# Kernel optimization log

Hardware: AMD Instinct MI355X
Metric: run time of the kernel (lower is better)

The kernel has to match this reference:

```python
import jax, jax.numpy as jnp
import numpy as np

IMG = 640
STRIDES = (8, 16, 32)
A = 5            # anchors per level
NC = 80          # num classes
IOU_TH = 0.5
NEG_RATIO = 1.0


def make_priors():
    scales = [1.0, 1.5, 2.0, 2.5, 3.0]
    out = []
    for s in STRIDES:
        f = IMG // s
        ys, xs = np.meshgrid(np.arange(f), np.arange(f), indexing='ij')
        cx = ((xs + 0.5) / f).ravel()
        cy = ((ys + 0.5) / f).ravel()
        for sc in scales:  # anchor-major to match merge_features (A, h, w) order
            wh = min(sc * 4.0 * s / IMG, 1.0)
            out.append(np.stack([cx, cy, np.full_like(cx, wh), np.full_like(cx, wh)], 1))
    return np.concatenate(out, 0).astype(np.float32)  # [42000, 4] cxcywh


def merge_features(feats):
    outs = []
    for feat in feats:
        n, c, h, w = feat.shape
        f = feat.reshape(n, A, c // A, h, w).transpose(0, 1, 3, 4, 2)
        outs.append(f.reshape(n, A * h * w, c // A))
    return jnp.concatenate(outs, axis=1)  # [n, M, 85]


def box_iou_cxcywh(a, b):
    # a [T,4], b [M,4] (cx,cy,w,h) -> IoU [T,M]
    a1 = jnp.concatenate([a[:, :2] - a[:, 2:] / 2, a[:, :2] + a[:, 2:] / 2], -1)
    b1 = jnp.concatenate([b[:, :2] - b[:, 2:] / 2, b[:, :2] + b[:, 2:] / 2], -1)
    tl = jnp.maximum(a1[:, None, :2], b1[None, :, :2])
    br = jnp.minimum(a1[:, None, 2:], b1[None, :, 2:])
    wh = jnp.clip(br - tl, 0.0)
    inter = wh[..., 0] * wh[..., 1]
    area_a = a[:, 2] * a[:, 3]
    area_b = b[:, 2] * b[:, 3]
    return inter / (area_a[:, None] + area_b[None, :] - inter + 1e-9)


def build_targets(targets, priors, batch):
    ious = box_iou_cxcywh(targets[:, 2:6], priors)  # [Nt, M]
    Nt, M = ious.shape
    img_ids = targets[:, 0].astype(jnp.int32)

    def per_image(i):
        valid = img_ids == i  # [Nt]
        iv = jnp.where(valid[:, None], ious, -1.0)
        best_gt_overlap = iv.max(0)            # [M]
        best_gt_idx = iv.argmax(0)             # [M]
        best_prior_idx = iv.argmax(1)          # [Nt]
        # torch: index_fill_(1) then sequential best_gt_overlap[best_prior_idx[j]] = j
        local_j = (jnp.cumsum(valid.astype(jnp.int32)) - 1).astype(jnp.float32)
        scat_idx = jnp.where(valid, best_prior_idx, M)  # drop invalid rows
        best_gt_overlap = best_gt_overlap.at[scat_idx].set(local_j, mode='drop')
        bbox = targets[best_gt_idx, 2:6]
        clss = targets[best_gt_idx, 1] + 1.0
        clss = jnp.where(best_gt_overlap < IOU_TH, 0.0, clss)
        t_xy = (bbox[:, :2] - priors[:, :2]) / priors[:, 2:]
        t_wh = jnp.log(bbox[:, 2:] / priors[:, 2:])
        return t_xy, t_wh, clss

    return jax.vmap(per_image)(jnp.arange(batch))  # [B,M,2],[B,M,2],[B,M]


def _smooth_l1(x):
    ax = jnp.abs(x)
    return jnp.where(ax < 1.0, 0.5 * ax * ax, ax - 0.5)


def compute_loss(preds, priors, targets):
    n, m, _ = preds.shape
    t_xy, t_wh, t_cls = build_targets(targets, priors, n)
    pos = t_cls > 0
    posf = pos.astype(preds.dtype)
    num_pos = posf.sum()

    # lbox: smooth L1 on xy and wh over positives (mean over pos*2 elements each)
    den2 = jnp.maximum(num_pos * 2.0, 1.0)
    lbox = (_smooth_l1(preds[..., 0:2] - t_xy) * posf[..., None]).sum() / den2 \
         + (_smooth_l1(preds[..., 2:4] - t_wh) * posf[..., None]).sum() / den2

    # lcls: cross entropy over positives, labels = t_cls - 1
    labels = jnp.clip(t_cls.astype(jnp.int32) - 1, 0, NC - 1)
    logz = jax.nn.log_softmax(preds[..., 5:], axis=-1)
    ce = -jnp.take_along_axis(logz, labels[..., None], axis=-1)[..., 0]
    lcls = (ce * posf).sum() / jnp.maximum(num_pos, 1.0)

    # hard negative mining (no grad): double argsort rank trick
    obj = preds[..., 4]
    loss_c = jax.lax.stop_gradient(-jax.nn.log_sigmoid(obj))
    loss_c = jnp.where(pos, 0.0, loss_c)
    order = jnp.argsort(-loss_c, axis=-1)
    rank = jnp.argsort(order, axis=-1)
    num_neg = jnp.minimum(NEG_RATIO * num_pos, m - num_pos)
    neg = rank.astype(preds.dtype) < num_neg
    sel = (pos | neg).astype(preds.dtype)

    # lobj: BCE-with-logits over pos|neg
    z = posf
    bce = jnp.maximum(obj, 0.0) - obj * z + jnp.log1p(jnp.exp(-jnp.abs(obj)))
    lobj = (bce * sel).sum() / jnp.maximum(sel.sum(), 1.0)

    loss = lbox + lcls + lobj
    return jnp.stack([loss, lbox, lobj, lcls])


def setup_inputs() -> dict:
    key = jax.random.key(0)
    ks = jax.random.split(key, 6)
    feat0 = jax.random.normal(ks[0], (8, 425, 80, 80), jnp.float32)
    feat1 = jax.random.normal(ks[1], (8, 425, 40, 40), jnp.float32)
    feat2 = jax.random.normal(ks[2], (8, 425, 20, 20), jnp.float32)
    B, T = 8, 20
    img = jnp.repeat(jnp.arange(B, dtype=jnp.float32), T)
    cls = jax.random.randint(ks[3], (B * T,), 0, NC).astype(jnp.float32)
    cxcy = jax.random.uniform(ks[4], (B * T, 2), minval=0.2, maxval=0.8)
    wh = jax.random.uniform(ks[5], (B * T, 2), minval=0.05, maxval=0.3)
    targets = jnp.concatenate([img[:, None], cls[:, None], cxcy, wh], 1)
    priors = jnp.asarray(make_priors())
    return {"feat0": feat0, "feat1": feat1, "feat2": feat2,
            "targets": targets, "priors": priors}


def reference(feat0, feat1, feat2, targets, priors):
    preds = merge_features([feat0, feat1, feat2])  # [8, 42000, 85]
    return compute_loss(preds, priors, targets)    # [loss, lbox, lobj, lcls]
```

## Files before the change

kernel.cpp:

```cpp
#include <hip/hip_runtime.h>
#include <math.h>

#define MTOT 42000
#define NB 8
#define NCLS 80
#define CAP_LIST 4096
#define MAXT 256
#define NT_MAX 2048
#define GX_MAIN 165
#define NBLK_MAIN (GX_MAIN*NB)
#define NBLK_SEL 1313
#define NCH 32
#define CS 1313

#define O_OVR 0
#define O_GIX (O_OVR + NB*MTOT*4)
#define O_LSC (O_GIX + NB*MTOT*4)
#define O_BCE (O_LSC + NB*MTOT*4)
#define O_BPI (O_BCE + NB*MTOT*4)
#define O_LJ  (O_BPI + NT_MAX*4)
#define O_LST (O_LJ + NT_MAX*4)
#define O_BPP (O_LST + NB*MAXT*4)
#define O_PA  (O_BPP + NT_MAX*NCH*8)
#define O_PN  (O_PA + NBLK_MAIN*16)
#define O_P2  (O_PN + NBLK_MAIN*4)
#define O_BINL (O_P2 + NBLK_SEL*8)
#define O_HA  (O_BINL + NB*CAP_LIST*2*4)
#define O_HB  (O_HA + NB*256*4)
#define O_ACC (O_HB + NB*256*4)
#define O_ACCI (O_ACC + 64)
#define O_CNT (O_ACCI + 256)
#define O_ZEND (O_CNT + 64)

__device__ __forceinline__ float iou_cxcywh(float acx,float acy,float aw,float ah,
                                            float bcx,float bcy,float bw,float bh){
  float ax0=acx-aw*0.5f, ay0=acy-ah*0.5f, ax1=acx+aw*0.5f, ay1=acy+ah*0.5f;
  float bx0=bcx-bw*0.5f, by0=bcy-bh*0.5f, bx1=bcx+bw*0.5f, by1=bcy+bh*0.5f;
  float tlx=fmaxf(ax0,bx0), tly=fmaxf(ay0,by0);
  float brx=fminf(ax1,bx1), bry=fminf(ay1,by1);
  float wx=fmaxf(brx-tlx,0.f), wy=fmaxf(bry-tly,0.f);
  float inter=wx*wy;
  return inter/(aw*ah+bw*bh-inter+1e-9f);
}

__device__ __forceinline__ float sl1(float x){
  float ax=fabsf(x); return ax<1.f ? 0.5f*ax*ax : ax-0.5f;
}

__device__ __forceinline__ void feat_base(const float* f0,const float* f1,const float* f2,
                                          int i,int m,const float** basep,int* hwp){
  const float* fp; int hw, loc;
  if(m<32000){ fp=f0; hw=6400; loc=m; }
  else if(m<40000){ fp=f1; hw=1600; loc=m-32000; }
  else { fp=f2; hw=400; loc=m-40000; }
  int a=loc/hw, p=loc-a*hw;
  *basep = fp + (size_t)(i*425 + a*85)*(size_t)hw + p;
  *hwp = hw;
}

__global__ void k_prep(const float* __restrict__ tg, int nt, int* __restrict__ list,
                       int* __restrict__ cnt, int* __restrict__ lj){
  int t=blockIdx.x*blockDim.x+threadIdx.x;
  if(t>=nt) return;
  int img=(int)tg[t*6];
  int j=0;
  for(int q=0;q<t;q++) if((int)tg[q*6]==img) j++;
  lj[t]=j;
  if(img>=0 && img<NB){
    atomicAdd(&cnt[img],1);
    if(j<MAXT) list[img*MAXT+j]=t;
  }
}

__global__ void k_match(const float* __restrict__ tg, const float* __restrict__ priors,
                        const int* __restrict__ list, const int* __restrict__ cnt,
                        float* __restrict__ ovr, int* __restrict__ gix){
  __shared__ float st[MAXT*6];
  __shared__ int   sidx[MAXT];
  int i = blockIdx.y;
  int n = min(cnt[i],MAXT);
  for(int j=threadIdx.x;j<n;j+=blockDim.x){
    int t=list[i*MAXT+j];
    sidx[j]=t;
    #pragma unroll
    for(int q=0;q<6;q++) st[j*6+q]=tg[t*6+q];
  }
  __syncthreads();
  int m = blockIdx.x*blockDim.x + threadIdx.x;
  if(m>=MTOT) return;
  float4 pr = ((const float4*)priors)[m];
  float maxv=-1.0f; int bi=0;
  for(int j=0;j<n;j++){
    float v=iou_cxcywh(st[j*6+2],st[j*6+3],st[j*6+4],st[j*6+5], pr.x,pr.y,pr.z,pr.w);
    if(v>maxv){ maxv=v; bi=sidx[j]; }
  }
  ovr[i*MTOT+m]=maxv; gix[i*MTOT+m]=bi;
}

__global__ void k_bpA(const float* __restrict__ tg, const float* __restrict__ priors,
                      int nt, unsigned long long* __restrict__ part){
  __shared__ unsigned long long s[256];
  int t=blockIdx.y; if(t>=nt) return;
  int c=blockIdx.x;
  float acx=tg[t*6+2],acy=tg[t*6+3],aw=tg[t*6+4],ah=tg[t*6+5];
  int m0=c*CS, m1=min(m0+CS,MTOT);
  float bv=-1.f; int bm=0;
  for(int m=m0+threadIdx.x;m<m1;m+=blockDim.x){
    float4 pr=((const float4*)priors)[m];
    float v=iou_cxcywh(acx,acy,aw,ah,pr.x,pr.y,pr.z,pr.w);
    if(v>bv){ bv=v; bm=m; }
  }
  unsigned long long p = (bv<0.f) ? 0ull
      : (((unsigned long long)__float_as_uint(bv))<<32) | (unsigned)(~bm);
  s[threadIdx.x]=p;
  __syncthreads();
  for(int o=128;o>0;o>>=1){
    if(threadIdx.x<o){ if(s[threadIdx.x+o]>s[threadIdx.x]) s[threadIdx.x]=s[threadIdx.x+o]; }
    __syncthreads();
  }
  if(threadIdx.x==0) part[(size_t)t*NCH+c]=s[0];
}

__global__ void k_bpB(const unsigned long long* __restrict__ part, int nt,
                      int* __restrict__ bpi){
  __shared__ unsigned long long s[64];
  int t=blockIdx.x; if(t>=nt) return;
  int l=threadIdx.x;
  s[l]=(l<NCH)? part[(size_t)t*NCH+l] : 0ull;
  __syncthreads();
  for(int o=32;o>0;o>>=1){
    if(l<o){ if(s[l+o]>s[l]) s[l]=s[l+o]; }
    __syncthreads();
  }
  if(l==0) bpi[t]=~((unsigned)(s[0]&0xFFFFFFFFull));
}

__global__ void k_scatter(const float* __restrict__ tg, int nt,
                          const int* __restrict__ bpi, const int* __restrict__ lj,
                          float* __restrict__ ovr){
  int t=blockIdx.x*blockDim.x+threadIdx.x;
  if(t>=nt) return;
  int img=(int)tg[t*6];
  if(img<0||img>=NB) return;
  int myp=bpi[t];
  for(int q=t+1;q<nt;q++)
    if((int)tg[q*6]==img && bpi[q]==myp) return;
  ovr[img*MTOT+myp]=(float)lj[t];
}

__global__ void k_main(const float* __restrict__ f0,const float* __restrict__ f1,const float* __restrict__ f2,
                       const float* __restrict__ tg,const float* __restrict__ priors,
                       const float* __restrict__ ovr,const int* __restrict__ gix,
                       float* __restrict__ lsc,float* __restrict__ bcearr,
                       unsigned* __restrict__ histA,
                       float4* __restrict__ partA,int* __restrict__ partN){
  __shared__ unsigned h[256];
  __shared__ float sxy[4],swh[4],sbp[4],sce[4];
  __shared__ int snp[4];
  int tid=threadIdx.x;
  h[tid]=0;
  __syncthreads();
  int i=blockIdx.y;
  int m=blockIdx.x*blockDim.x+tid;
  int lane=tid&63, wid=tid>>6;
  bool valid=(m<MTOT);

  float lxy=0.f,lwh=0.f,bcep=0.f; int npos=0; bool pos=false; int gi=0;
  if(valid){
    int gid=i*MTOT+m;
    const float* base; int hw;
    feat_base(f0,f1,f2,i,m,&base,&hw);
    float ov=ovr[gid]; gi=gix[gid];
    float tc=tg[gi*6+1]+1.0f;
    pos=(ov>=0.5f)&&(tc>0.f);
    float obj=base[(size_t)4*hw];
    float sp=log1pf(expf(-fabsf(obj)));
    float bce=fmaxf(obj,0.f)-(pos?obj:0.f)+sp;
    float lc=pos?0.f:(fmaxf(-obj,0.f)+sp);
    lsc[gid]=lc; bcearr[gid]=bce;
    atomicAdd(&h[__float_as_uint(lc)>>24],1u);
    if(pos){
      npos=1; bcep=bce;
      float4 pr=((const float4*)priors)[m];
      float bx=tg[gi*6+2],by=tg[gi*6+3],bw=tg[gi*6+4],bh=tg[gi*6+5];
      float tx=(bx-pr.x)/pr.z, ty=(by-pr.y)/pr.w;
      float tw=logf(bw/pr.z), th=logf(bh/pr.w);
      lxy=sl1(base[0]-tx)+sl1(base[(size_t)hw]-ty);
      lwh=sl1(base[(size_t)2*hw]-tw)+sl1(base[(size_t)3*hw]-th);
    }
  }

  float wce=0.f;
  unsigned long long mask=__ballot(valid&&pos);
  while(mask){
    int s=__ffsll(mask)-1;
    mask&=mask-1;
    int m_s=__shfl(m,s);
    int gi_s=__shfl(gi,s);
    const float* bs; int hws;
    feat_base(f0,f1,f2,i,m_s,&bs,&hws);
    int label=(int)(tg[gi_s*6+1]+1.0f)-1;
    label=min(NCLS-1,max(0,label));
    float v0=bs[(size_t)(5+lane)*hws];
    float v1=(lane<16)?bs[(size_t)(69+lane)*hws]:-3.0e38f;
    float mx=fmaxf(v0,v1);
    #pragma unroll
    for(int o=32;o>0;o>>=1) mx=fmaxf(mx,__shfl_xor(mx,o));
    float se=expf(v0-mx)+((lane<16)?expf(v1-mx):0.f);
    float xl=((lane==label)?v0:0.f)+((lane<16&&lane+64==label)?v1:0.f);
    #pragma unroll
    for(int o=32;o>0;o>>=1){ se+=__shfl_xor(se,o); xl+=__shfl_xor(xl,o); }
    wce+=logf(se)+mx-xl;
  }

  #pragma unroll
  for(int o=32;o>0;o>>=1){
    lxy+=__shfl_xor(lxy,o); lwh+=__shfl_xor(lwh,o);
    bcep+=__shfl_xor(bcep,o); npos+=__shfl_xor(npos,o);
  }
  if(lane==0){ sxy[wid]=lxy; swh[wid]=lwh; sbp[wid]=bcep; sce[wid]=wce; snp[wid]=npos; }
  __syncthreads();
  unsigned c=h[tid];
  if(c) atomicAdd(&histA[i*256+tid],c);
  if(tid==0){
    float4 pa;
    pa.x=sxy[0]+sxy[1]+sxy[2]+sxy[3];
    pa.y=swh[0]+swh[1]+swh[2]+swh[3];
    pa.z=sce[0]+sce[1]+sce[2]+sce[3];
    pa.w=sbp[0]+sbp[1]+sbp[2]+sbp[3];
    int bid=blockIdx.y*gridDim.x+blockIdx.x;
    partA[bid]=pa;
    partN[bid]=snp[0]+snp[1]+snp[2]+snp[3];
  }
}

__global__ void k_red(const float4* __restrict__ partA,const int* __restrict__ partN,
                      float* __restrict__ accf,int* __restrict__ acci){
  __shared__ float a0[256],a1[256],a2[256],a3[256]; __shared__ int an[256];
  int t=threadIdx.x;
  float x=0,y=0,z=0,w=0; int n=0;
  for(int b=t;b<NBLK_MAIN;b+=256){
    float4 p=partA[b]; x+=p.x; y+=p.y; z+=p.z; w+=p.w; n+=partN[b];
  }
  a0[t]=x; a1[t]=y; a2[t]=z; a3[t]=w; an[t]=n;
  __syncthreads();
  for(int o=128;o>0;o>>=1){
    if(t<o){ a0[t]+=a0[t+o]; a1[t]+=a1[t+o]; a2[t]+=a2[t+o]; a3[t]+=a3[t+o]; an[t]+=an[t+o]; }
    __syncthreads();
  }
  if(t==0){ accf[0]=a0[0]; accf[1]=a1[0]; accf[2]=a2[0]; accf[3]=a3[0]; acci[0]=an[0]; }
}

__global__ void k_scanA(const unsigned* __restrict__ histA, int* __restrict__ acci){
  int i=blockIdx.x;
  __shared__ unsigned a[256];
  a[threadIdx.x]=histA[i*256+threadIdx.x];
  __syncthreads();
  if(threadIdx.x==0){
    int np=acci[0];
    int k=min(np, MTOT-np);
    if(k<=0){ acci[2+i]=0x7fffffff; acci[10+i]=0; return; }
    int run=0;
    for(int c=255;c>=0;c--){
      int cb=(int)a[c];
      if(run<k && run+cb>=k){ acci[2+i]=c; acci[10+i]=k-run; return; }
      run+=cb;
    }
    acci[2+i]=0; acci[10+i]=k-run;
  }
}

__global__ void k_histB(const float* __restrict__ lsc, const int* __restrict__ acci,
                        unsigned* __restrict__ histB){
  __shared__ unsigned h[256];
  h[threadIdx.x]=0;
  __syncthreads();
  int i=blockIdx.y;
  int ca=acci[2+i];
  int m=blockIdx.x*blockDim.x+threadIdx.x;
  if(m<MTOT && ca!=0x7fffffff){
    unsigned u=__float_as_uint(lsc[i*MTOT+m]);
    if((int)(u>>24)==ca) atomicAdd(&h[(u>>16)&0xFF],1u);
  }
  __syncthreads();
  unsigned c=h[threadIdx.x];
  if(c) atomicAdd(&histB[i*256+threadIdx.x],c);
}

__global__ void k_scanB(const unsigned* __restrict__ histB, int* __restrict__ acci){
  int i=blockIdx.x;
  __shared__ unsigned a[256];
  a[threadIdx.x]=histB[i*256+threadIdx.x];
  __syncthreads();
  if(threadIdx.x==0){
    int ca=acci[2+i], kres=acci[10+i];
    if(ca==0x7fffffff || kres<=0){ acci[2+i]=0x7fffffff; acci[10+i]=0; return; }
    int run=0;
    for(int f=255;f>=0;f--){
      int cb=(int)a[f];
      if(run<kres && run+cb>=kres){ acci[2+i]=(ca<<8)|f; acci[10+i]=kres-run; return; }
      run+=cb;
    }
    acci[2+i]=(ca<<8); acci[10+i]=kres-run;
  }
}

__global__ void k_select(const float* __restrict__ lsc,const float* __restrict__ bcearr,
                         int* __restrict__ acci,float2* __restrict__ part2,
                         int* __restrict__ binlist){
  __shared__ float ss[4]; __shared__ float sc[4];
  int tid=threadIdx.x, lane=tid&63, wid=tid>>6;
  int gid=blockIdx.x*blockDim.x+tid;
  float s=0.f, c=0.f;
  if(gid<NB*MTOT){
    int i=gid/MTOT;
    int bs_=acci[2+i];
    unsigned u=__float_as_uint(lsc[gid]);
    int bin=(int)(u>>16);
    if(bin>bs_){ s=bcearr[gid]; c=1.f; }
    else if(bin==bs_){
      int idx=atomicAdd(&acci[18+i],1);
      if(idx<CAP_LIST){
        binlist[((size_t)i*CAP_LIST+idx)*2  ]=(int)u;
        binlist[((size_t)i*CAP_LIST+idx)*2+1]=gid;
      }
    }
  }
  #pragma unroll
  for(int o=32;o>0;o>>=1){ s+=__shfl_xor(s,o); c+=__shfl_xor(c,o); }
  if(lane==0){ ss[wid]=s; sc[wid]=c; }
  __syncthreads();
  if(tid==0) part2[blockIdx.x]=make_float2(ss[0]+ss[1]+ss[2]+ss[3], sc[0]+sc[1]+sc[2]+sc[3]);
}

__global__ void k_ties(const float* __restrict__ bcearr,int* __restrict__ acci,
                       float* __restrict__ accf,const int* __restrict__ binlist){
  int i=blockIdx.x;
  if(acci[2+i]==0x7fffffff) return;
  int n=min(acci[18+i],CAP_LIST);
  int r=acci[10+i];
  for(int e=threadIdx.x;e<n;e+=blockDim.x){
    unsigned ue=(unsigned)binlist[((size_t)i*CAP_LIST+e)*2];
    int ge=binlist[((size_t)i*CAP_LIST+e)*2+1];
    int rank=0;
    for(int q=0;q<n;q++){
      unsigned uq=(unsigned)binlist[((size_t)i*CAP_LIST+q)*2];
      int gq=binlist[((size_t)i*CAP_LIST+q)*2+1];
      rank += ((uq>ue) || (uq==ue && gq<ge)) ? 1 : 0;
    }
    if(rank<r){
      atomicAdd(&accf[5], bcearr[ge]);
      atomicAdd(&acci[1], 1);
    }
  }
}

__global__ void k_final(const float* __restrict__ accf,const int* __restrict__ acci,
                        const float2* __restrict__ part2,float* __restrict__ out){
  __shared__ float ssum[256]; __shared__ float scnt[256];
  int t=threadIdx.x;
  float s=0.f,c=0.f;
  for(int b=t;b<NBLK_SEL;b+=256){ float2 p=part2[b]; s+=p.x; c+=p.y; }
  ssum[t]=s; scnt[t]=c;
  __syncthreads();
  for(int o=128;o>0;o>>=1){
    if(t<o){ ssum[t]+=ssum[t+o]; scnt[t]+=scnt[t+o]; }
    __syncthreads();
  }
  if(t==0){
    int np=acci[0];
    float npf=(float)np;
    float den2=fmaxf(2.f*npf,1.f);
    float lbox=accf[0]/den2 + accf[1]/den2;
    float lcls=accf[2]/fmaxf(npf,1.f);
    float negsum=ssum[0]+accf[5];
    float negcnt=scnt[0]+(float)acci[1];
    float selc=npf+negcnt;
    float lobj=(accf[3]+negsum)/fmaxf(selc,1.f);
    out[0]=lbox+lcls+lobj;
    out[1]=lbox;
    out[2]=lobj;
    out[3]=lcls;
  }
}

extern "C" void kernel_launch(void* const* d_in, const int* in_sizes, int n_in,
                              void* d_out, int out_size, void* d_ws, size_t ws_size,
                              hipStream_t stream) {
  const float* f0=(const float*)d_in[0];
  const float* f1=(const float*)d_in[1];
  const float* f2=(const float*)d_in[2];
  const float* tg=(const float*)d_in[3];
  const float* priors=(const float*)d_in[4];
  int nt = in_sizes[3]/6;
  if(nt>NT_MAX) nt=NT_MAX;

  char* ws=(char*)d_ws;
  float*    ovr    =(float*)   (ws+O_OVR);
  int*      gix    =(int*)     (ws+O_GIX);
  float*    lsc    =(float*)   (ws+O_LSC);
  float*    bcearr =(float*)   (ws+O_BCE);
  int*      bpi    =(int*)     (ws+O_BPI);
  int*      lj     =(int*)     (ws+O_LJ);
  int*      list   =(int*)     (ws+O_LST);
  unsigned long long* bpp=(unsigned long long*)(ws+O_BPP);
  float4*   partA  =(float4*)  (ws+O_PA);
  int*      partN  =(int*)     (ws+O_PN);
  float2*   part2  =(float2*)  (ws+O_P2);
  int*      binlist=(int*)     (ws+O_BINL);
  unsigned* histA  =(unsigned*)(ws+O_HA);
  unsigned* histB  =(unsigned*)(ws+O_HB);
  float*    accf   =(float*)   (ws+O_ACC);
  int*      acci   =(int*)     (ws+O_ACCI);
  int*      cnt    =(int*)     (ws+O_CNT);

  hipMemsetAsync(ws+O_HA, 0, (size_t)(O_ZEND-O_HA), stream);

  int ntb=(nt+255)/256;
  k_prep<<<ntb,256,0,stream>>>(tg,nt,list,cnt,lj);
  dim3 gm(GX_MAIN, NB);
  k_match<<<gm,256,0,stream>>>(tg,priors,list,cnt,ovr,gix);
  dim3 gbp(NCH, nt);
  k_bpA<<<gbp,256,0,stream>>>(tg,priors,nt,bpp);
  k_bpB<<<nt,64,0,stream>>>(bpp,nt,bpi);
  k_scatter<<<ntb,256,0,stream>>>(tg,nt,bpi,lj,ovr);
  k_main<<<gm,256,0,stream>>>(f0,f1,f2,tg,priors,ovr,gix,lsc,bcearr,histA,partA,partN);
  k_red<<<1,256,0,stream>>>(partA,partN,accf,acci);
  k_scanA<<<NB,256,0,stream>>>(histA,acci);
  k_histB<<<gm,256,0,stream>>>(lsc,acci,histB);
  k_scanB<<<NB,256,0,stream>>>(histB,acci);
  k_select<<<NBLK_SEL,256,0,stream>>>(lsc,bcearr,acci,part2,binlist);
  k_ties<<<NB,256,0,stream>>>(bcearr,acci,accf,binlist);
  k_final<<<1,256,0,stream>>>(accf,acci,part2,(float*)d_out);
}
```

Measured before the change: 158.9 us.

## Fuse small launch-bound kernels and fold memset into init kernel

Result: faster. 151.5 us (-4.7%).

```diff
diff --git a/kernel.cpp b/kernel.cpp
--- a/kernel.cpp
+++ b/kernel.cpp
@@ -9,7 +9,6 @@
 #define NT_MAX 2048
 #define GX_MAIN 165
 #define NBLK_MAIN (GX_MAIN*NB)
-#define NBLK_SEL 1313
 #define NCH 32
 #define CS 1313
 
@@ -24,13 +23,15 @@
 #define O_PA  (O_BPP + NT_MAX*NCH*8)
 #define O_PN  (O_PA + NBLK_MAIN*16)
 #define O_P2  (O_PN + NBLK_MAIN*4)
-#define O_BINL (O_P2 + NBLK_SEL*8)
-#define O_HA  (O_BINL + NB*CAP_LIST*2*4)
+#define O_BINL (O_P2 + NBLK_MAIN*8)
+#define O_CNT (O_BINL + NB*CAP_LIST*2*4)
+#define O_HA  (((O_CNT + NB*4 + 255)/256)*256)
 #define O_HB  (O_HA + NB*256*4)
 #define O_ACC (O_HB + NB*256*4)
 #define O_ACCI (O_ACC + 64)
-#define O_CNT (O_ACCI + 256)
-#define O_ZEND (O_CNT + 64)
+#define O_ZEND (O_ACCI + 256)
+#define ZWORDS ((O_ZEND - O_HA)/4)
+#define ZBLK ((ZWORDS + 255)/256)
 
 __device__ __forceinline__ float iou_cxcywh(float acx,float acy,float aw,float ah,
                                             float bcx,float bcy,float bw,float bh){
@@ -58,18 +59,27 @@
   *hwp = hw;
 }
 
-__global__ void k_prep(const float* __restrict__ tg, int nt, int* __restrict__ list,
-                       int* __restrict__ cnt, int* __restrict__ lj){
-  int t=blockIdx.x*blockDim.x+threadIdx.x;
+__global__ void k_init(const float* __restrict__ tg, int nt, int* __restrict__ list,
+                       int* __restrict__ cnt, int* __restrict__ lj,
+                       unsigned* __restrict__ zbase){
+  int bx=blockIdx.x, tid=threadIdx.x;
+  if(bx<ZBLK){
+    int w=bx*256+tid;
+    if(w<ZWORDS) zbase[w]=0u;
+    return;
+  }
+  if(bx==ZBLK && tid<NB){
+    int c=0;
+    for(int q=0;q<nt;q++) if((int)tg[q*6]==tid) c++;
+    cnt[tid]=c;
+  }
+  int t=(bx-ZBLK)*256+tid;
   if(t>=nt) return;
   int img=(int)tg[t*6];
   int j=0;
   for(int q=0;q<t;q++) if((int)tg[q*6]==img) j++;
   lj[t]=j;
-  if(img>=0 && img<NB){
-    atomicAdd(&cnt[img],1);
-    if(j<MAXT) list[img*MAXT+j]=t;
-  }
+  if(img>=0 && img<NB && j<MAXT) list[img*MAXT+j]=t;
 }
 
 __global__ void k_match(const float* __restrict__ tg, const float* __restrict__ priors,
@@ -234,30 +244,34 @@
   }
 }
 
-__global__ void k_red(const float4* __restrict__ partA,const int* __restrict__ partN,
-                      float* __restrict__ accf,int* __restrict__ acci){
-  __shared__ float a0[256],a1[256],a2[256],a3[256]; __shared__ int an[256];
-  int t=threadIdx.x;
-  float x=0,y=0,z=0,w=0; int n=0;
+__global__ void k_redscanA(const float4* __restrict__ partA,const int* __restrict__ partN,
+                           const unsigned* __restrict__ histA,
+                           float* __restrict__ accf,int* __restrict__ acci){
+  __shared__ int an[256];
+  __shared__ float a0[256],a1[256],a2[256],a3[256];
+  __shared__ unsigned a[256];
+  int t=threadIdx.x, i=blockIdx.x;
+  bool lead=(i==0);
+  int n=0; float x=0,y=0,z=0,w=0;
   for(int b=t;b<NBLK_MAIN;b+=256){
-    float4 p=partA[b]; x+=p.x; y+=p.y; z+=p.z; w+=p.w; n+=partN[b];
-  }
-  a0[t]=x; a1[t]=y; a2[t]=z; a3[t]=w; an[t]=n;
+    n+=partN[b];
+    if(lead){ float4 p=partA[b]; x+=p.x; y+=p.y; z+=p.z; w+=p.w; }
+  }
+  an[t]=n;
+  if(lead){ a0[t]=x; a1[t]=y; a2[t]=z; a3[t]=w; }
   __syncthreads();
   for(int o=128;o>0;o>>=1){
-    if(t<o){ a0[t]+=a0[t+o]; a1[t]+=a1[t+o]; a2[t]+=a2[t+o]; a3[t]+=a3[t+o]; an[t]+=an[t+o]; }
+    if(t<o){
+      an[t]+=an[t+o];
+      if(lead){ a0[t]+=a0[t+o]; a1[t]+=a1[t+o]; a2[t]+=a2[t+o]; a3[t]+=a3[t+o]; }
+    }
     __syncthreads();
   }
-  if(t==0){ accf[0]=a0[0]; accf[1]=a1[0]; accf[2]=a2[0]; accf[3]=a3[0]; acci[0]=an[0]; }
-}
-
-__global__ void k_scanA(const unsigned* __restrict__ histA, int* __restrict__ acci){
-  int i=blockIdx.x;
-  __shared__ unsigned a[256];
-  a[threadIdx.x]=histA[i*256+threadIdx.x];
-  __syncthreads();
-  if(threadIdx.x==0){
-    int np=acci[0];
+  int np=an[0];
+  if(lead && t==0){ accf[0]=a0[0]; accf[1]=a1[0]; accf[2]=a2[0]; accf[3]=a3[0]; acci[0]=np; }
+  a[t]=histA[i*256+t];
+  __syncthreads();
+  if(t==0){
     int k=min(np, MTOT-np);
     if(k<=0){ acci[2+i]=0x7fffffff; acci[10+i]=0; return; }
     int run=0;
@@ -287,34 +301,37 @@
   if(c) atomicAdd(&histB[i*256+threadIdx.x],c);
 }
 
-__global__ void k_scanB(const unsigned* __restrict__ histB, int* __restrict__ acci){
-  int i=blockIdx.x;
-  __shared__ unsigned a[256];
-  a[threadIdx.x]=histB[i*256+threadIdx.x];
-  __syncthreads();
-  if(threadIdx.x==0){
-    int ca=acci[2+i], kres=acci[10+i];
-    if(ca==0x7fffffff || kres<=0){ acci[2+i]=0x7fffffff; acci[10+i]=0; return; }
-    int run=0;
-    for(int f=255;f>=0;f--){
-      int cb=(int)a[f];
-      if(run<kres && run+cb>=kres){ acci[2+i]=(ca<<8)|f; acci[10+i]=kres-run; return; }
-      run+=cb;
-    }
-    acci[2+i]=(ca<<8); acci[10+i]=kres-run;
-  }
+__device__ __forceinline__ void fine_scan(const unsigned* hb,int ca,int kres,int* bs_out,int* r_out){
+  if(ca==0x7fffffff){ *bs_out=0x7fffffff; *r_out=0; return; }
+  int run=0, bs=-1, r=0;
+  for(int f=255;f>=0;f--){
+    int cb=(int)hb[f];
+    if(run<kres && run+cb>=kres){ bs=(ca<<8)|f; r=kres-run; break; }
+    run+=cb;
+  }
+  if(bs<0){ bs=(ca<<8); r=kres-run; }
+  *bs_out=bs; *r_out=r;
 }
 
 __global__ void k_select(const float* __restrict__ lsc,const float* __restrict__ bcearr,
+                         const unsigned* __restrict__ histB,
                          int* __restrict__ acci,float2* __restrict__ part2,
                          int* __restrict__ binlist){
+  __shared__ unsigned hb[256];
+  __shared__ int sbs;
   __shared__ float ss[4]; __shared__ float sc[4];
   int tid=threadIdx.x, lane=tid&63, wid=tid>>6;
-  int gid=blockIdx.x*blockDim.x+tid;
+  int i=blockIdx.y;
+  int ca=acci[2+i], kres=acci[10+i];
+  hb[tid]=(ca==0x7fffffff)?0u:histB[i*256+tid];
+  __syncthreads();
+  if(tid==0){ int bs,r; fine_scan(hb,ca,kres,&bs,&r); sbs=bs; }
+  __syncthreads();
+  int bs_=sbs;
+  int m=blockIdx.x*blockDim.x+tid;
   float s=0.f, c=0.f;
-  if(gid<NB*MTOT){
-    int i=gid/MTOT;
-    int bs_=acci[2+i];
+  if(m<MTOT){
+    int gid=i*MTOT+m;
     unsigned u=__float_as_uint(lsc[gid]);
     int bin=(int)(u>>16);
     if(bin>bs_){ s=bcearr[gid]; c=1.f; }
@@ -330,16 +347,24 @@
   for(int o=32;o>0;o>>=1){ s+=__shfl_xor(s,o); c+=__shfl_xor(c,o); }
   if(lane==0){ ss[wid]=s; sc[wid]=c; }
   __syncthreads();
-  if(tid==0) part2[blockIdx.x]=make_float2(ss[0]+ss[1]+ss[2]+ss[3], sc[0]+sc[1]+sc[2]+sc[3]);
+  if(tid==0) part2[blockIdx.y*gridDim.x+blockIdx.x]=make_float2(ss[0]+ss[1]+ss[2]+ss[3], sc[0]+sc[1]+sc[2]+sc[3]);
 }
 
 __global__ void k_ties(const float* __restrict__ bcearr,int* __restrict__ acci,
-                       float* __restrict__ accf,const int* __restrict__ binlist){
-  int i=blockIdx.x;
-  if(acci[2+i]==0x7fffffff) return;
+                       float* __restrict__ accf,const int* __restrict__ binlist,
+                       const unsigned* __restrict__ histB){
+  __shared__ unsigned hb[256];
+  __shared__ int sbs, sr;
+  int i=blockIdx.x, tid=threadIdx.x;
+  int ca=acci[2+i], kres=acci[10+i];
+  hb[tid]=(ca==0x7fffffff)?0u:histB[i*256+tid];
+  __syncthreads();
+  if(tid==0){ int bs,r; fine_scan(hb,ca,kres,&bs,&r); sbs=bs; sr=r; }
+  __syncthreads();
+  if(sbs==0x7fffffff) return;
   int n=min(acci[18+i],CAP_LIST);
-  int r=acci[10+i];
-  for(int e=threadIdx.x;e<n;e+=blockDim.x){
+  int r=sr;
+  for(int e=tid;e<n;e+=blockDim.x){
     unsigned ue=(unsigned)binlist[((size_t)i*CAP_LIST+e)*2];
     int ge=binlist[((size_t)i*CAP_LIST+e)*2+1];
     int rank=0;
@@ -360,7 +385,7 @@
   __shared__ float ssum[256]; __shared__ float scnt[256];
   int t=threadIdx.x;
   float s=0.f,c=0.f;
-  for(int b=t;b<NBLK_SEL;b+=256){ float2 p=part2[b]; s+=p.x; c+=p.y; }
+  for(int b=t;b<NBLK_MAIN;b+=256){ float2 p=part2[b]; s+=p.x; c+=p.y; }
   ssum[t]=s; scnt[t]=c;
   __syncthreads();
   for(int o=128;o>0;o>>=1){
@@ -408,16 +433,15 @@
   int*      partN  =(int*)     (ws+O_PN);
   float2*   part2  =(float2*)  (ws+O_P2);
   int*      binlist=(int*)     (ws+O_BINL);
+  int*      cnt    =(int*)     (ws+O_CNT);
   unsigned* histA  =(unsigned*)(ws+O_HA);
   unsigned* histB  =(unsigned*)(ws+O_HB);
   float*    accf   =(float*)   (ws+O_ACC);
   int*      acci   =(int*)     (ws+O_ACCI);
-  int*      cnt    =(int*)     (ws+O_CNT);
-
-  hipMemsetAsync(ws+O_HA, 0, (size_t)(O_ZEND-O_HA), stream);
+  unsigned* zbase  =(unsigned*)(ws+O_HA);
 
   int ntb=(nt+255)/256;
-  k_prep<<<ntb,256,0,stream>>>(tg,nt,list,cnt,lj);
+  k_init<<<ZBLK+ntb,256,0,stream>>>(tg,nt,list,cnt,lj,zbase);
   dim3 gm(GX_MAIN, NB);
   k_match<<<gm,256,0,stream>>>(tg,priors,list,cnt,ovr,gix);
   dim3 gbp(NCH, nt);
@@ -425,11 +449,9 @@
   k_bpB<<<nt,64,0,stream>>>(bpp,nt,bpi);
   k_scatter<<<ntb,256,0,stream>>>(tg,nt,bpi,lj,ovr);
   k_main<<<gm,256,0,stream>>>(f0,f1,f2,tg,priors,ovr,gix,lsc,bcearr,histA,partA,partN);
-  k_red<<<1,256,0,stream>>>(partA,partN,accf,acci);
-  k_scanA<<<NB,256,0,stream>>>(histA,acci);
+  k_redscanA<<<NB,256,0,stream>>>(partA,partN,histA,accf,acci);
   k_histB<<<gm,256,0,stream>>>(lsc,acci,histB);
-  k_scanB<<<NB,256,0,stream>>>(histB,acci);
-  k_select<<<NBLK_SEL,256,0,stream>>>(lsc,bcearr,acci,part2,binlist);
-  k_ties<<<NB,256,0,stream>>>(bcearr,acci,accf,binlist);
+  k_select<<<gm,256,0,stream>>>(lsc,bcearr,histB,acci,part2,binlist);
+  k_ties<<<NB,256,0,stream>>>(bcearr,acci,accf,binlist,histB);
   k_final<<<1,256,0,stream>>>(accf,acci,part2,(float*)d_out);
 }
```
